# Kernel tuning notes

Hardware: AMD Instinct MI355X
Metric: run time of the kernel (lower is better)

Reference implementation:

```python
import jax, jax.numpy as jnp
import numpy as np

COV_EMB = 32
N_HEAD = 2
FACTOR_TCL = 2   # TemporalConvolutionalLayer factor (default 2)
FACTOR_MLP = 1   # MLP factor passed from MultiAttention init
EPS = 1e-5


def _conv1d_causal(x, w, b):
    # x: [N, C, T], w: [O, C, 3]; torch pads 2 both sides then slices [..., :-2],
    # equivalent to left-pad 2 only -> output length T.
    y = jax.lax.conv_general_dilated(x, w, window_strides=(1,), padding=[(2, 0)],
                                     dimension_numbers=('NCH', 'OIH', 'NCH'))
    return y + b[None, :, None]


def _tcl(x, w_conv, b_conv, w_proj, b_proj):
    # TemporalConvolutionalLayer: x [..., T, C] -> [..., T, C]
    shp = x.shape
    T, C = shp[-2], shp[-1]
    x2 = x.reshape(-1, T, C).transpose(0, 2, 1)              # [N, C, T]
    h = jax.nn.gelu(_conv1d_causal(x2, w_conv, b_conv), approximate=False)
    h = h.transpose(0, 2, 1)                                  # [N, T, 2C]
    out = h @ w_proj.T + b_proj                               # [N, T, C]
    return out.reshape(*shp[:-1], C)


def _layernorm(x, w):
    mu = jnp.mean(x, axis=-1, keepdims=True)
    var = jnp.var(x, axis=-1, keepdims=True)
    return (x - mu) * jax.lax.rsqrt(var + EPS) * w


def setup_inputs() -> dict:
    key = jax.random.key(0)
    ks = jax.random.split(key, 20)
    C = COV_EMB
    C2 = FACTOR_TCL * C
    s = 0.02
    inp = {
        'causal_decoder': jax.random.normal(ks[0], (8, 4, 1024, C), jnp.float32),
        'past_kv': jax.random.normal(ks[1], (8, 1024, C), jnp.float32),
    }
    def tcl_params(i):
        return (jax.random.normal(ks[i], (C2, C, 3), jnp.float32) * s,
                jnp.zeros((C2,), jnp.float32),
                jax.random.normal(ks[i + 1], (C, C2), jnp.float32) * s,
                jnp.zeros((C,), jnp.float32))
    inp['wq_conv'], inp['bq_conv'], inp['wq_proj'], inp['bq_proj'] = tcl_params(2)
    inp['wk_conv'], inp['bk_conv'], inp['wk_proj'], inp['bk_proj'] = tcl_params(4)
    inp['wv_conv'], inp['bv_conv'], inp['wv_proj'], inp['bv_proj'] = tcl_params(6)
    inp['w_cproj'] = jax.random.normal(ks[8], (C, C), jnp.float32) * s   # bias=False
    inp['ln_w'] = jnp.ones((C,), jnp.float32)                            # bias=False
    inp['w_fc'] = jax.random.normal(ks[9], (FACTOR_MLP * C, C), jnp.float32) * s   # bias=False
    inp['w_mlp_proj'] = jax.random.normal(ks[10], (C, FACTOR_MLP * C), jnp.float32) * s
    return inp


def reference(causal_decoder, past_kv,
              wq_conv, bq_conv, wq_proj, bq_proj,
              wk_conv, bk_conv, wk_proj, bk_proj,
              wv_conv, bv_conv, wv_proj, bv_proj,
              w_cproj, ln_w, w_fc, w_mlp_proj):
    B, F, T, C = causal_decoder.shape
    nh, hd = N_HEAD, C // N_HEAD

    q = _tcl(causal_decoder, wq_conv, bq_conv, wq_proj, bq_proj)   # [B,F,T,C]
    k = _tcl(past_kv, wk_conv, bk_conv, wk_proj, bk_proj)          # [B,S,C]
    v = _tcl(past_kv, wv_conv, bv_conv, wv_proj, bv_proj)          # [B,S,C]

    S = k.shape[1]
    q = q.reshape(B, F, T, nh, hd).transpose(0, 1, 3, 2, 4)        # [B,F,h,T,d]
    k = k.reshape(B, S, nh, hd).transpose(0, 2, 1, 3)              # [B,h,S,d]
    v = v.reshape(B, S, nh, hd).transpose(0, 2, 1, 3)              # [B,h,S,d]

    scale = 1.0 / jnp.sqrt(jnp.asarray(hd, q.dtype))
    scores = jnp.einsum('bfhtd,bhsd->bfhts', q, k) * scale          # [B,F,h,T,S]
    attn = jax.nn.softmax(scores, axis=-1)
    y = jnp.einsum('bfhts,bhsd->bfhtd', attn, v)                    # [B,F,h,T,d]
    y = y.transpose(0, 1, 3, 2, 4).reshape(B, F, T, C)

    out = causal_decoder + y @ w_cproj.T                            # resid_dropout = id (p=0)
    h = _layernorm(out, ln_w)
    mlp = jax.nn.gelu(h @ w_fc.T, approximate=False) @ w_mlp_proj.T
    out = out + mlp
    return out
```

## Files before the change

kernel.cpp:

```cpp
#include <hip/hip_runtime.h>
#include <hip/hip_bf16.h>

#define T_LEN 1024

typedef __attribute__((ext_vector_type(8))) short short8;
typedef __attribute__((ext_vector_type(4))) short short4v;
typedef __attribute__((ext_vector_type(4))) float float4v;

__device__ __forceinline__ float gelu_exact(float x) {
    return 0.5f * x * (1.0f + erff(x * 0.70710678118654752440f));
}
__device__ __forceinline__ unsigned short f2bf(float f) {
    unsigned u = __float_as_uint(f);
    u += 0x7fffu + ((u >> 16) & 1u);
    return (unsigned short)(u >> 16);
}
__device__ __forceinline__ unsigned pk2bf(float a, float b) {
    __hip_bfloat162 h = __float22bfloat162_rn(make_float2(a, b));
    unsigned u;
    __builtin_memcpy(&u, &h, 4);
    return u;
}

__global__ __launch_bounds__(256) void kv_tcl(
    const float* __restrict__ pkv,
    const float* __restrict__ wkc, const float* __restrict__ bkc,
    const float* __restrict__ wkp, const float* __restrict__ bkp,
    const float* __restrict__ wvc, const float* __restrict__ bvc,
    const float* __restrict__ wvp, const float* __restrict__ bvp,
    unsigned short* __restrict__ kbf, unsigned short* __restrict__ vtbf)
{
    __shared__ __align__(16) unsigned short Abuf[32 * 96];
    __shared__ __align__(16) unsigned short WbT[64 * 96];
    __shared__ __align__(16) unsigned short Hb[32 * 72];
    __shared__ __align__(16) unsigned short WpB[32 * 72];

    const int tid = threadIdx.x;
    const int gb = blockIdx.x;

    const float *wc, *bc, *wp, *bp;
    unsigned short* outb;
    int n, mode;
    if (gb < 256) { n = gb >> 5;         wc = wkc; bc = bkc; wp = wkp; bp = bkp; outb = kbf;  mode = 0; }
    else          { n = (gb - 256) >> 5; wc = wvc; bc = bvc; wp = wvp; bp = bvp; outb = vtbf; mode = 1; }
    const int t0 = (gb & 31) * 32;

#pragma unroll
    for (int it = 0; it < 3; ++it) {
        int s = (tid + it * 256) >> 3;
        int sub = tid & 7;
        int t = s / 3, tap = s - t * 3;
        int tau = t0 + t - 2 + tap;
        float4 xv = make_float4(0.f, 0.f, 0.f, 0.f);
        if (tau >= 0) xv = *(const float4*)&pkv[((size_t)n * T_LEN + tau) * 32 + sub * 4];
        short4v pk = { (short)f2bf(xv.x), (short)f2bf(xv.y),
                       (short)f2bf(xv.z), (short)f2bf(xv.w) };
        *(short4v*)&Abuf[t * 96 + tap * 32 + sub * 4] = pk;
    }
#pragma unroll
    for (int it = 0; it < 6; ++it) {
        int i4 = tid + it * 256;
        int idx = i4 * 4;
        int o = idx / 96, r = idx - o * 96;
        float4 w4 = *(const float4*)&wc[idx];
        float we[4] = { w4.x, w4.y, w4.z, w4.w };
#pragma unroll
        for (int e = 0; e < 4; ++e) {
            int re = r + e, c = re / 3, tap = re - c * 3;
            WbT[o * 96 + tap * 32 + c] = f2bf(we[e]);
        }
    }
#pragma unroll
    for (int it = 0; it < 2; ++it) {
        int i4 = tid + it * 256;
        int idx = i4 * 4;
        int c = idx >> 6, o = idx & 63;
        float4 w4 = *(const float4*)&wp[idx];
        short4v pk = { (short)f2bf(w4.x), (short)f2bf(w4.y),
                       (short)f2bf(w4.z), (short)f2bf(w4.w) };
        *(short4v*)&WpB[c * 72 + o] = pk;
    }

    const int w = tid >> 6;
    const int ln = tid & 63;
    const int sn = ln & 15;
    const int quad = ln >> 4;

    const float bcv = bc[w * 16 + sn];
    const int tmw = w & 1, cnw = w >> 1;
    const float bpv = bp[cnw * 16 + sn];

    __syncthreads();

    short8 b0 = *(const short8*)&WbT[(w * 16 + sn) * 96 + 0  + quad * 8];
    short8 b1 = *(const short8*)&WbT[(w * 16 + sn) * 96 + 32 + quad * 8];
    short8 b2 = *(const short8*)&WbT[(w * 16 + sn) * 96 + 64 + quad * 8];
    float4v zero = { 0.f, 0.f, 0.f, 0.f };
    float4v acc[2] = { zero, zero };
#pragma unroll
    for (int tm = 0; tm < 2; ++tm) {
        const unsigned short* ar = &Abuf[(tm * 16 + sn) * 96 + quad * 8];
        short8 a0 = *(const short8*)(ar + 0);
        short8 a1 = *(const short8*)(ar + 32);
        short8 a2 = *(const short8*)(ar + 64);
        acc[tm] = __builtin_amdgcn_mfma_f32_16x16x32_bf16(a0, b0, acc[tm], 0, 0, 0);
        acc[tm] = __builtin_amdgcn_mfma_f32_16x16x32_bf16(a1, b1, acc[tm], 0, 0, 0);
        acc[tm] = __builtin_amdgcn_mfma_f32_16x16x32_bf16(a2, b2, acc[tm], 0, 0, 0);
    }
#pragma unroll
    for (int tm = 0; tm < 2; ++tm) {
        float ge[4];
        ge[0] = gelu_exact(acc[tm].x + bcv);
        ge[1] = gelu_exact(acc[tm].y + bcv);
        ge[2] = gelu_exact(acc[tm].z + bcv);
        ge[3] = gelu_exact(acc[tm].w + bcv);
#pragma unroll
        for (int i = 0; i < 4; ++i)
            Hb[(tm * 16 + quad * 4 + i) * 72 + w * 16 + sn] = f2bf(ge[i]);
    }

    __syncthreads();

    const unsigned short* hr = &Hb[(tmw * 16 + sn) * 72 + quad * 8];
    short8 pa0 = *(const short8*)(hr + 0);
    short8 pa1 = *(const short8*)(hr + 32);
    short8 pb0 = *(const short8*)&WpB[(cnw * 16 + sn) * 72 + quad * 8];
    short8 pb1 = *(const short8*)&WpB[(cnw * 16 + sn) * 72 + 32 + quad * 8];
    float4v pacc = zero;
    pacc = __builtin_amdgcn_mfma_f32_16x16x32_bf16(pa0, pb0, pacc, 0, 0, 0);
    pacc = __builtin_amdgcn_mfma_f32_16x16x32_bf16(pa1, pb1, pacc, 0, 0, 0);

    float v[4] = { pacc.x + bpv, pacc.y + bpv, pacc.z + bpv, pacc.w + bpv };
#pragma unroll
    for (int i = 0; i < 4; ++i) {
        int t = tmw * 16 + quad * 4 + i;
        int c = cnw * 16 + sn;
        if (mode == 0) {
            outb[((size_t)n * T_LEN + t0 + t) * 32 + c] = f2bf(v[i]);
        } else {
            outb[((size_t)(n * 2 + cnw) * 16 + sn) * T_LEN + t0 + t] = f2bf(v[i]);
        }
    }
}

__global__ __launch_bounds__(512) void fused_qae(
    const float* __restrict__ cd,
    const float* __restrict__ wqc, const float* __restrict__ bqc,
    const float* __restrict__ wqp, const float* __restrict__ bqp,
    const unsigned short* __restrict__ kbf,
    const unsigned short* __restrict__ vtbf,
    const float* __restrict__ wcp, const float* __restrict__ lnw,
    const float* __restrict__ wfc, const float* __restrict__ wmp,
    float* __restrict__ out)
{
    __shared__ __align__(16) char smem[43520];
    unsigned short* Abuf = (unsigned short*)(smem);
    unsigned short* WbT  = (unsigned short*)(smem + 12288);
    unsigned short* Hb   = (unsigned short*)(smem + 24576);
    unsigned short* WpB  = (unsigned short*)(smem + 33792);
    unsigned short* qs   = (unsigned short*)(smem + 38400);
    unsigned short* plds = (unsigned short*)(smem);

    const int tid = threadIdx.x;
    const int bf = blockIdx.x >> 4;
    const int tt = blockIdx.x & 15;
    const int t0 = tt * 64;
    const int b = bf >> 2;
    const float SC = 0.36067376022224085f;

#pragma unroll
    for (int it = 0; it < 3; ++it) {
        int idx = tid + it * 512;
        int s = idx >> 3;
        int sub = idx & 7;
        int t = s / 3, tap = s - t * 3;
        int tau = t0 + t - 2 + tap;
        float4 xv = make_float4(0.f, 0.f, 0.f, 0.f);
        if (tau >= 0) xv = *(const float4*)&cd[((size_t)bf * T_LEN + tau) * 32 + sub * 4];
        short4v pk = { (short)f2bf(xv.x), (short)f2bf(xv.y),
                       (short)f2bf(xv.z), (short)f2bf(xv.w) };
        *(short4v*)&Abuf[t * 96 + tap * 32 + sub * 4] = pk;
    }
#pragma unroll
    for (int it = 0; it < 3; ++it) {
        int i4 = tid + it * 512;
        int idx = i4 * 4;
        int o = idx / 96, r = idx - o * 96;
        float4 w4 = *(const float4*)&wqc[idx];
        float we[4] = { w4.x, w4.y, w4.z, w4.w };
#pragma unroll
        for (int e = 0; e < 4; ++e) {
            int re = r + e, c = re / 3, tap = re - c * 3;
            WbT[o * 96 + tap * 32 + c] = f2bf(we[e]);
        }
    }
    {
        int idx = tid * 4;
        int c = idx >> 6, o = idx & 63;
        float4 w4 = *(const float4*)&wqp[idx];
        short4v pk = { (short)f2bf(w4.x), (short)f2bf(w4.y),
                       (short)f2bf(w4.z), (short)f2bf(w4.w) };
        *(short4v*)&WpB[c * 72 + o] = pk;
    }

    const int w = tid >> 6;
    const int ln = tid & 63;
    const int sn = ln & 15;
    const int quad = ln >> 4;
    const float4v zero = { 0.f, 0.f, 0.f, 0.f };

    __syncthreads();

    {
        const int tm = w & 3;
        const int on0 = w >> 2, on1 = on0 + 2;
        const unsigned short* ar = &Abuf[(tm * 16 + sn) * 96 + quad * 8];
        short8 a0 = *(const short8*)(ar + 0);
        short8 a1 = *(const short8*)(ar + 32);
        short8 a2 = *(const short8*)(ar + 64);
        const unsigned short* br0 = &WbT[(on0 * 16 + sn) * 96 + quad * 8];
        const unsigned short* br1 = &WbT[(on1 * 16 + sn) * 96 + quad * 8];
        float4v c0 = zero, c1 = zero;
        c0 = __builtin_amdgcn_mfma_f32_16x16x32_bf16(a0, *(const short8*)(br0 + 0),  c0, 0, 0, 0);
        c0 = __builtin_amdgcn_mfma_f32_16x16x32_bf16(a1, *(const short8*)(br0 + 32), c0, 0, 0, 0);
        c0 = __builtin_amdgcn_mfma_f32_16x16x32_bf16(a2, *(const short8*)(br0 + 64), c0, 0, 0, 0);
        c1 = __builtin_amdgcn_mfma_f32_16x16x32_bf16(a0, *(const short8*)(br1 + 0),  c1, 0, 0, 0);
        c1 = __builtin_amdgcn_mfma_f32_16x16x32_bf16(a1, *(const short8*)(br1 + 32), c1, 0, 0, 0);
        c1 = __builtin_amdgcn_mfma_f32_16x16x32_bf16(a2, *(const short8*)(br1 + 64), c1, 0, 0, 0);
        const float bc0 = bqc[on0 * 16 + sn], bc1 = bqc[on1 * 16 + sn];
        float g0[4] = { gelu_exact(c0.x + bc0), gelu_exact(c0.y + bc0),
                        gelu_exact(c0.z + bc0), gelu_exact(c0.w + bc0) };
        float g1[4] = { gelu_exact(c1.x + bc1), gelu_exact(c1.y + bc1),
                        gelu_exact(c1.z + bc1), gelu_exact(c1.w + bc1) };
#pragma unroll
        for (int i = 0; i < 4; ++i) {
            Hb[(tm * 16 + quad * 4 + i) * 72 + on0 * 16 + sn] = f2bf(g0[i]);
            Hb[(tm * 16 + quad * 4 + i) * 72 + on1 * 16 + sn] = f2bf(g1[i]);
        }
    }
    __syncthreads();

    {
        const int tm = w & 3, cn = w >> 2;
        const unsigned short* hr = &Hb[(tm * 16 + sn) * 72 + quad * 8];
        short8 pa0 = *(const short8*)(hr + 0);
        short8 pa1 = *(const short8*)(hr + 32);
        const unsigned short* wr_ = &WpB[(cn * 16 + sn) * 72 + quad * 8];
        short8 pb0 = *(const short8*)(wr_ + 0);
        short8 pb1 = *(const short8*)(wr_ + 32);
        float4v pacc = zero;
        pacc = __builtin_amdgcn_mfma_f32_16x16x32_bf16(pa0, pb0, pacc, 0, 0, 0);
        pacc = __builtin_amdgcn_mfma_f32_16x16x32_bf16(pa1, pb1, pacc, 0, 0, 0);
        const float bpv = bqp[cn * 16 + sn];
        float v[4] = { (pacc.x + bpv) * SC, (pacc.y + bpv) * SC,
                       (pacc.z + bpv) * SC, (pacc.w + bpv) * SC };
#pragma unroll
        for (int i = 0; i < 4; ++i)
            qs[(tm * 16 + quad * 4 + i) * 40 + cn * 16 + sn] = f2bf(v[i]);
    }
    __syncthreads();

    const int h = w & 1, rt = w >> 1;
    short8 aq = {0, 0, 0, 0, 0, 0, 0, 0};
    if (quad < 2)
        aq = *(const short8*)&qs[(rt * 16 + sn) * 40 + h * 16 + quad * 8];

    const unsigned short* kb = kbf + (size_t)b * T_LEN * 32 + h * 16 + quad * 8;
    const unsigned short* vb = vtbf + ((size_t)(b * 2 + h) * 16 + sn) * T_LEN + quad * 8;
    unsigned short* pwA = plds + w * 1152;
    unsigned short* pwB = pwA + 576;

    float4v yacc = zero;
    float l0 = 0.f, l1 = 0.f, l2 = 0.f, l3 = 0.f;

#pragma unroll 1
    for (int s0 = 0; s0 < 1024; s0 += 64) {
        short8 ka0 = {0,0,0,0,0,0,0,0}, ka1 = ka0, kb0 = ka0, kb1 = ka0;
        if (quad < 2) {
            ka0 = *(const short8*)(kb + (size_t)(s0 + sn) * 32);
            ka1 = *(const short8*)(kb + (size_t)(s0 + 16 + sn) * 32);
            kb0 = *(const short8*)(kb + (size_t)(s0 + 32 + sn) * 32);
            kb1 = *(const short8*)(kb + (size_t)(s0 + 48 + sn) * 32);
        }
        short8 bvA = *(const short8*)(vb + s0);
        short8 bvB = *(const short8*)(vb + s0 + 32);

        float4v cA0 = __builtin_amdgcn_mfma_f32_16x16x32_bf16(aq, ka0, zero, 0, 0, 0);
        float4v cA1 = __builtin_amdgcn_mfma_f32_16x16x32_bf16(aq, ka1, zero, 0, 0, 0);
        float4v cB0 = __builtin_amdgcn_mfma_f32_16x16x32_bf16(aq, kb0, zero, 0, 0, 0);
        float4v cB1 = __builtin_amdgcn_mfma_f32_16x16x32_bf16(aq, kb1, zero, 0, 0, 0);

        float a0x = exp2f(cA0.x), a0y = exp2f(cA0.y), a0z = exp2f(cA0.z), a0w = exp2f(cA0.w);
        float a1x = exp2f(cA1.x), a1y = exp2f(cA1.y), a1z = exp2f(cA1.z), a1w = exp2f(cA1.w);
        float b0x = exp2f(cB0.x), b0y = exp2f(cB0.y), b0z = exp2f(cB0.z), b0w = exp2f(cB0.w);
        float b1x = exp2f(cB1.x), b1y = exp2f(cB1.y), b1z = exp2f(cB1.z), b1w = exp2f(cB1.w);

        l0 += (a0x + a1x) + (b0x + b1x);
        l1 += (a0y + a1y) + (b0y + b1y);
        l2 += (a0z + a1z) + (b0z + b1z);
        l3 += (a0w + a1w) + (b0w + b1w);

        const int tb = quad * 4;
        unsigned uA0 = pk2bf(a0x, a1x), uA1 = pk2bf(a0y, a1y);
        unsigned uA2 = pk2bf(a0z, a1z), uA3 = pk2bf(a0w, a1w);
        unsigned uB0 = pk2bf(b0x, b1x), uB1 = pk2bf(b0y, b1y);
        unsigned uB2 = pk2bf(b0z, b1z), uB3 = pk2bf(b0w, b1w);
        pwA[(tb + 0) * 36 + sn]      = (unsigned short)uA0;
        pwA[(tb + 0) * 36 + 16 + sn] = (unsigned short)(uA0 >> 16);
        pwA[(tb + 1) * 36 + sn]      = (unsigned short)uA1;
        pwA[(tb + 1) * 36 + 16 + sn] = (unsigned short)(uA1 >> 16);
        pwA[(tb + 2) * 36 + sn]      = (unsigned short)uA2;
        pwA[(tb + 2) * 36 + 16 + sn] = (unsigned short)(uA2 >> 16);
        pwA[(tb + 3) * 36 + sn]      = (unsigned short)uA3;
        pwA[(tb + 3) * 36 + 16 + sn] = (unsigned short)(uA3 >> 16);
        pwB[(tb + 0) * 36 + sn]      = (unsigned short)uB0;
        pwB[(tb + 0) * 36 + 16 + sn] = (unsigned short)(uB0 >> 16);
        pwB[(tb + 1) * 36 + sn]      = (unsigned short)uB1;
        pwB[(tb + 1) * 36 + 16 + sn] = (unsigned short)(uB1 >> 16);
        pwB[(tb + 2) * 36 + sn]      = (unsigned short)uB2;
        pwB[(tb + 2) * 36 + 16 + sn] = (unsigned short)(uB2 >> 16);
        pwB[(tb + 3) * 36 + sn]      = (unsigned short)uB3;
        pwB[(tb + 3) * 36 + 16 + sn] = (unsigned short)(uB3 >> 16);

        const unsigned short* prA = pwA + sn * 36 + quad * 8;
        const unsigned short* prB = pwB + sn * 36 + quad * 8;
        short4v aloA = *(const short4v*)prA;
        short4v ahiA = *(const short4v*)(prA + 4);
        short4v aloB = *(const short4v*)prB;
        short4v ahiB = *(const short4v*)(prB + 4);
        short8 apA = {aloA.x, aloA.y, aloA.z, aloA.w, ahiA.x, ahiA.y, ahiA.z, ahiA.w};
        short8 apB = {aloB.x, aloB.y, aloB.z, aloB.w, ahiB.x, ahiB.y, ahiB.z, ahiB.w};

        yacc = __builtin_amdgcn_mfma_f32_16x16x32_bf16(apA, bvA, yacc, 0, 0, 0);
        yacc = __builtin_amdgcn_mfma_f32_16x16x32_bf16(apB, bvB, yacc, 0, 0, 0);
    }

#pragma unroll
    for (int off = 1; off < 16; off <<= 1) {
        l0 += __shfl_xor(l0, off); l1 += __shfl_xor(l1, off);
        l2 += __shfl_xor(l2, off); l3 += __shfl_xor(l3, off);
    }

    float* sy = (float*)(smem + 24576);
    {
        const float i0 = 1.f / l0, i1 = 1.f / l1, i2 = 1.f / l2, i3 = 1.f / l3;
        const int r0 = rt * 16 + quad * 4;
        sy[(r0 + 0) * 32 + h * 16 + sn] = yacc.x * i0;
        sy[(r0 + 1) * 32 + h * 16 + sn] = yacc.y * i1;
        sy[(r0 + 2) * 32 + h * 16 + sn] = yacc.z * i2;
        sy[(r0 + 3) * 32 + h * 16 + sn] = yacc.w * i3;
    }
    __syncthreads();

    float* swc = (float*)(smem + 0);
    float* swf = (float*)(smem + 4608);
    float* swm = (float*)(smem + 9216);
    float* sln = (float*)(smem + 13824);
    float* shn = (float*)(smem + 13952);
    float* sgv = (float*)(smem + 16256);
    for (int i = tid; i < 1024; i += 512) {
        int r = i >> 5, cc = i & 31;
        swc[r * 36 + cc] = wcp[i];
        swf[r * 36 + cc] = wfc[i];
        swm[r * 36 + cc] = wmp[i];
    }
    if (tid < 32) sln[tid] = lnw[tid];
    __syncthreads();

    const int rl = tid >> 5, c = tid & 31;
    const float lnwc = sln[c];
#pragma unroll 1
    for (int p = 0; p < 4; ++p) {
        int r = p * 16 + rl;
        size_t row = (size_t)bf * T_LEN + t0 + r;
        float x1 = cd[row * 32 + c];
#pragma unroll
        for (int j4 = 0; j4 < 8; ++j4) {
            float4 yv = *(const float4*)&sy[r * 32 + j4 * 4];
            const float* wv = &swc[c * 36 + j4 * 4];
            x1 += wv[0] * yv.x + wv[1] * yv.y + wv[2] * yv.z + wv[3] * yv.w;
        }
        float s1 = x1, s2 = x1 * x1;
#pragma unroll
        for (int off = 16; off; off >>= 1) {
            s1 += __shfl_xor(s1, off);
            s2 += __shfl_xor(s2, off);
        }
        float mu = s1 * (1.0f / 32.0f);
        float var = s2 * (1.0f / 32.0f) - mu * mu;
        float hn = (x1 - mu) * rsqrtf(var + 1e-5f) * lnwc;
        shn[rl * 36 + c] = hn;
        float ga = 0.f;
#pragma unroll
        for (int j4 = 0; j4 < 8; ++j4) {
            float4 hv = *(const float4*)&shn[rl * 36 + j4 * 4];
            const float* wv = &swf[c * 36 + j4 * 4];
            ga += wv[0] * hv.x + wv[1] * hv.y + wv[2] * hv.z + wv[3] * hv.w;
        }
        float gv = gelu_exact(ga);
        sgv[rl * 36 + c] = gv;
        float oa = x1;
#pragma unroll
        for (int j4 = 0; j4 < 8; ++j4) {
            float4 gvv = *(const float4*)&sgv[rl * 36 + j4 * 4];
            const float* wv = &swm[c * 36 + j4 * 4];
            oa += wv[0] * gvv.x + wv[1] * gvv.y + wv[2] * gvv.z + wv[3] * gvv.w;
        }
        out[row * 32 + c] = oa;
    }
}

extern "C" void kernel_launch(void* const* d_in, const int* in_sizes, int n_in,
                              void* d_out, int out_size, void* d_ws, size_t ws_size,
                              hipStream_t stream) {
    const float* cd  = (const float*)d_in[0];
    const float* pkv = (const float*)d_in[1];
    const float* wqc = (const float*)d_in[2];
    const float* bqc = (const float*)d_in[3];
    const float* wqp = (const float*)d_in[4];
    const float* bqp = (const float*)d_in[5];
    const float* wkc = (const float*)d_in[6];
    const float* bkc = (const float*)d_in[7];
    const float* wkp = (const float*)d_in[8];
    const float* bkp = (const float*)d_in[9];
    const float* wvc = (const float*)d_in[10];
    const float* bvc = (const float*)d_in[11];
    const float* wvp = (const float*)d_in[12];
    const float* bvp = (const float*)d_in[13];
    const float* wcp = (const float*)d_in[14];
    const float* lnw = (const float*)d_in[15];
    const float* wfc = (const float*)d_in[16];
    const float* wmp = (const float*)d_in[17];

    unsigned short* kbf  = (unsigned short*)d_ws;
    unsigned short* vtbf = kbf + (size_t)8 * 1024 * 32;

    kv_tcl<<<512, 256, 0, stream>>>(pkv, wkc, bkc, wkp, bkp,
                                    wvc, bvc, wvp, bvp, kbf, vtbf);
    fused_qae<<<512, 512, 0, stream>>>(cd, wqc, bqc, wqp, bqp, kbf, vtbf,
                                       wcp, lnw, wfc, wmp, (float*)d_out);
}
```

Measured before the change: 132.1 us.

## Halve query tile per block and split attention keys across wave halves

```diff
diff --git a/kernel.cpp b/kernel.cpp
--- a/kernel.cpp
+++ b/kernel.cpp
@@ -153,33 +153,35 @@
     const float* __restrict__ wfc, const float* __restrict__ wmp,
     float* __restrict__ out)
 {
-    __shared__ __align__(16) char smem[43520];
+    __shared__ __align__(16) char smem[30208];
     unsigned short* Abuf = (unsigned short*)(smem);
-    unsigned short* WbT  = (unsigned short*)(smem + 12288);
-    unsigned short* Hb   = (unsigned short*)(smem + 24576);
-    unsigned short* WpB  = (unsigned short*)(smem + 33792);
-    unsigned short* qs   = (unsigned short*)(smem + 38400);
+    unsigned short* WbT  = (unsigned short*)(smem + 6144);
+    unsigned short* Hb   = (unsigned short*)(smem + 18432);
+    unsigned short* WpB  = (unsigned short*)(smem + 23040);
+    unsigned short* qs   = (unsigned short*)(smem + 27648);
     unsigned short* plds = (unsigned short*)(smem);
 
     const int tid = threadIdx.x;
-    const int bf = blockIdx.x >> 4;
-    const int tt = blockIdx.x & 15;
-    const int t0 = tt * 64;
+    const int bf = blockIdx.x >> 5;
+    const int tt = blockIdx.x & 31;
+    const int t0 = tt * 32;
     const int b = bf >> 2;
     const float SC = 0.36067376022224085f;
 
 #pragma unroll
-    for (int it = 0; it < 3; ++it) {
+    for (int it = 0; it < 2; ++it) {
         int idx = tid + it * 512;
-        int s = idx >> 3;
-        int sub = idx & 7;
-        int t = s / 3, tap = s - t * 3;
-        int tau = t0 + t - 2 + tap;
-        float4 xv = make_float4(0.f, 0.f, 0.f, 0.f);
-        if (tau >= 0) xv = *(const float4*)&cd[((size_t)bf * T_LEN + tau) * 32 + sub * 4];
-        short4v pk = { (short)f2bf(xv.x), (short)f2bf(xv.y),
-                       (short)f2bf(xv.z), (short)f2bf(xv.w) };
-        *(short4v*)&Abuf[t * 96 + tap * 32 + sub * 4] = pk;
+        if (idx < 768) {
+            int s = idx >> 3;
+            int sub = idx & 7;
+            int t = s / 3, tap = s - t * 3;
+            int tau = t0 + t - 2 + tap;
+            float4 xv = make_float4(0.f, 0.f, 0.f, 0.f);
+            if (tau >= 0) xv = *(const float4*)&cd[((size_t)bf * T_LEN + tau) * 32 + sub * 4];
+            short4v pk = { (short)f2bf(xv.x), (short)f2bf(xv.y),
+                           (short)f2bf(xv.z), (short)f2bf(xv.w) };
+            *(short4v*)&Abuf[t * 96 + tap * 32 + sub * 4] = pk;
+        }
     }
 #pragma unroll
     for (int it = 0; it < 3; ++it) {
@@ -212,36 +214,27 @@
     __syncthreads();
 
     {
-        const int tm = w & 3;
-        const int on0 = w >> 2, on1 = on0 + 2;
+        const int tm = w & 1, on = w >> 1;
         const unsigned short* ar = &Abuf[(tm * 16 + sn) * 96 + quad * 8];
         short8 a0 = *(const short8*)(ar + 0);
         short8 a1 = *(const short8*)(ar + 32);
         short8 a2 = *(const short8*)(ar + 64);
-        const unsigned short* br0 = &WbT[(on0 * 16 + sn) * 96 + quad * 8];
-        const unsigned short* br1 = &WbT[(on1 * 16 + sn) * 96 + quad * 8];
-        float4v c0 = zero, c1 = zero;
-        c0 = __builtin_amdgcn_mfma_f32_16x16x32_bf16(a0, *(const short8*)(br0 + 0),  c0, 0, 0, 0);
-        c0 = __builtin_amdgcn_mfma_f32_16x16x32_bf16(a1, *(const short8*)(br0 + 32), c0, 0, 0, 0);
-        c0 = __builtin_amdgcn_mfma_f32_16x16x32_bf16(a2, *(const short8*)(br0 + 64), c0, 0, 0, 0);
-        c1 = __builtin_amdgcn_mfma_f32_16x16x32_bf16(a0, *(const short8*)(br1 + 0),  c1, 0, 0, 0);
-        c1 = __builtin_amdgcn_mfma_f32_16x16x32_bf16(a1, *(const short8*)(br1 + 32), c1, 0, 0, 0);
-        c1 = __builtin_amdgcn_mfma_f32_16x16x32_bf16(a2, *(const short8*)(br1 + 64), c1, 0, 0, 0);
-        const float bc0 = bqc[on0 * 16 + sn], bc1 = bqc[on1 * 16 + sn];
+        const unsigned short* br = &WbT[(on * 16 + sn) * 96 + quad * 8];
+        float4v c0 = zero;
+        c0 = __builtin_amdgcn_mfma_f32_16x16x32_bf16(a0, *(const short8*)(br + 0),  c0, 0, 0, 0);
+        c0 = __builtin_amdgcn_mfma_f32_16x16x32_bf16(a1, *(const short8*)(br + 32), c0, 0, 0, 0);
+        c0 = __builtin_amdgcn_mfma_f32_16x16x32_bf16(a2, *(const short8*)(br + 64), c0, 0, 0, 0);
+        const float bc0 = bqc[on * 16 + sn];
         float g0[4] = { gelu_exact(c0.x + bc0), gelu_exact(c0.y + bc0),
                         gelu_exact(c0.z + bc0), gelu_exact(c0.w + bc0) };
-        float g1[4] = { gelu_exact(c1.x + bc1), gelu_exact(c1.y + bc1),
-                        gelu_exact(c1.z + bc1), gelu_exact(c1.w + bc1) };
-#pragma unroll
-        for (int i = 0; i < 4; ++i) {
-            Hb[(tm * 16 + quad * 4 + i) * 72 + on0 * 16 + sn] = f2bf(g0[i]);
-            Hb[(tm * 16 + quad * 4 + i) * 72 + on1 * 16 + sn] = f2bf(g1[i]);
-        }
-    }
-    __syncthreads();
-
-    {
-        const int tm = w & 3, cn = w >> 2;
+#pragma unroll
+        for (int i = 0; i < 4; ++i)
+            Hb[(tm * 16 + quad * 4 + i) * 72 + on * 16 + sn] = f2bf(g0[i]);
+    }
+    __syncthreads();
+
+    if (w < 4) {
+        const int tm = w & 1, cn = w >> 1;
         const unsigned short* hr = &Hb[(tm * 16 + sn) * 72 + quad * 8];
         short8 pa0 = *(const short8*)(hr + 0);
         short8 pa1 = *(const short8*)(hr + 32);
@@ -260,7 +253,7 @@
     }
     __syncthreads();
 
-    const int h = w & 1, rt = w >> 1;
+    const int h = w & 1, rt = (w >> 1) & 1, sh = w >> 2;
     short8 aq = {0, 0, 0, 0, 0, 0, 0, 0};
     if (quad < 2)
         aq = *(const short8*)&qs[(rt * 16 + sn) * 40 + h * 16 + quad * 8];
@@ -272,9 +265,10 @@
 
     float4v yacc = zero;
     float l0 = 0.f, l1 = 0.f, l2 = 0.f, l3 = 0.f;
+    const int sbeg = sh * 512;
 
 #pragma unroll 1
-    for (int s0 = 0; s0 < 1024; s0 += 64) {
+    for (int s0 = sbeg; s0 < sbeg + 512; s0 += 64) {
         short8 ka0 = {0,0,0,0,0,0,0,0}, ka1 = ka0, kb0 = ka0, kb1 = ka0;
         if (quad < 2) {
             ka0 = *(const short8*)(kb + (size_t)(s0 + sn) * 32);
@@ -341,8 +335,28 @@
         l2 += __shfl_xor(l2, off); l3 += __shfl_xor(l3, off);
     }
 
-    float* sy = (float*)(smem + 24576);
-    {
+    float* pbuf = (float*)(smem + 18432);
+    float* lbuf = (float*)(smem + 22528);
+    float* sy   = (float*)(smem + 22784);
+    const int wj = w & 3;
+    if (sh == 1) {
+        *(float4*)(pbuf + wj * 256 + ln * 4) =
+            make_float4(yacc.x, yacc.y, yacc.z, yacc.w);
+        if (sn == 0) {
+            lbuf[wj * 16 + quad * 4 + 0] = l0;
+            lbuf[wj * 16 + quad * 4 + 1] = l1;
+            lbuf[wj * 16 + quad * 4 + 2] = l2;
+            lbuf[wj * 16 + quad * 4 + 3] = l3;
+        }
+    }
+    __syncthreads();
+    if (sh == 0) {
+        float4 o = *(float4*)(pbuf + wj * 256 + ln * 4);
+        yacc.x += o.x; yacc.y += o.y; yacc.z += o.z; yacc.w += o.w;
+        l0 += lbuf[wj * 16 + quad * 4 + 0];
+        l1 += lbuf[wj * 16 + quad * 4 + 1];
+        l2 += lbuf[wj * 16 + quad * 4 + 2];
+        l3 += lbuf[wj * 16 + quad * 4 + 3];
         const float i0 = 1.f / l0, i1 = 1.f / l1, i2 = 1.f / l2, i3 = 1.f / l3;
         const int r0 = rt * 16 + quad * 4;
         sy[(r0 + 0) * 32 + h * 16 + sn] = yacc.x * i0;
@@ -350,7 +364,6 @@
         sy[(r0 + 2) * 32 + h * 16 + sn] = yacc.z * i2;
         sy[(r0 + 3) * 32 + h * 16 + sn] = yacc.w * i3;
     }
-    __syncthreads();
 
     float* swc = (float*)(smem + 0);
     float* swf = (float*)(smem + 4608);
@@ -370,7 +383,7 @@
     const int rl = tid >> 5, c = tid & 31;
     const float lnwc = sln[c];
 #pragma unroll 1
-    for (int p = 0; p < 4; ++p) {
+    for (int p = 0; p < 2; ++p) {
         int r = p * 16 + rl;
         size_t row = (size_t)bf * T_LEN + t0 + r;
         float x1 = cd[row * 32 + c];
@@ -437,6 +450,6 @@
 
     kv_tcl<<<512, 256, 0, stream>>>(pkv, wkc, bkc, wkp, bkp,
                                     wvc, bvc, wvp, bvp, kbf, vtbf);
-    fused_qae<<<512, 512, 0, stream>>>(cd, wqc, bqc, wqp, bqp, kbf, vtbf,
-                                       wcp, lnw, wfc, wmp, (float*)d_out);
-}
+    fused_qae<<<1024, 512, 0, stream>>>(cd, wqc, bqc, wqp, bqp, kbf, vtbf,
+                                        wcp, lnw, wfc, wmp, (float*)d_out);
+}
```

Result: no change. 133.5 us (+1.1%).
